# Performance work log

Measured on AMD Instinct MI355X. Metric: run time of the kernel, lower is better.

Reference implementation:

```python
import jax, jax.numpy as jnp
import numpy as np

B, G, N, E, F, H = 16, 8, 512, 8192, 128, 128
BN_EPS = 1e-5


def setup_inputs() -> dict:
    key = jax.random.key(0)
    ks = jax.random.split(key, 6)
    feats = jax.random.normal(ks[0], (B, G, N, F), jnp.float32)
    edges = jax.random.randint(ks[1], (B, G, 2, E), 0, N, dtype=jnp.int32)
    s = lambda k, shape: jax.random.normal(k, shape, jnp.float32) * 0.05
    return {
        "feats": feats,
        "edges": edges,
        "W0": s(ks[2], (F, H)), "b0": jnp.zeros((H,), jnp.float32),
        "W1": s(ks[3], (H, H)), "b1": jnp.zeros((H,), jnp.float32),
        "Wt": s(ks[4], (H, H)), "bt": jnp.zeros((H,), jnp.float32),
        "gamma": jnp.ones((H,), jnp.float32),
        "beta": jnp.zeros((H,), jnp.float32),
        "run_mean": jnp.zeros((H,), jnp.float32),
        "run_var": jnp.ones((H,), jnp.float32),
    }


def _gconv(x, src, dst, W, b):
    # DGL GraphConv with norm='both': relu(D_in^{-1/2} A D_out^{-1/2} X W + b)
    ones = jnp.ones(src.shape, jnp.float32)
    out_deg = jnp.clip(jax.ops.segment_sum(ones, src, num_segments=N), 1.0)
    in_deg = jnp.clip(jax.ops.segment_sum(ones, dst, num_segments=N), 1.0)
    h = x * jax.lax.rsqrt(out_deg)[:, None]          # src normalization
    agg = jax.ops.segment_sum(h[src], dst, num_segments=N)  # SpMM gather+scatter
    h = agg * jax.lax.rsqrt(in_deg)[:, None]          # dst normalization
    return jax.nn.relu(h @ W + b)


def reference(feats, edges, W0, b0, W1, b1, Wt, bt, gamma, beta, run_mean, run_var):
    def per_graph(x, e):
        src, dst = e[0], e[1]
        h = _gconv(x, src, dst, W0, b0)
        h = _gconv(h, src, dst, W1, b1)
        emb = h.mean(axis=0)  # dgl.mean_nodes readout -> [H]
        z = emb @ Wt + bt
        # BatchNorm1d in eval mode (batch of 1 graph embedding)
        z = gamma * (z - run_mean) * jax.lax.rsqrt(run_var + BN_EPS) + beta
        return jax.nn.relu(z)

    xf = feats.reshape(B * G, N, F)
    ef = edges.reshape(B * G, 2, E)
    out = jax.vmap(per_graph)(xf, ef)  # [B*G, H]
    # torch.stack nesting gives (batch, n_graph, 1, H) since mean_nodes returns [1, H]
    return out.reshape(B, G, 1, H)
```

## Files before the change

### kernel.cpp

```cpp
#include <hip/hip_runtime.h>
#include <hip/hip_bf16.h>

#define NN 512
#define NE 8192
#define NG 128
#define FH 128
#define APITCH 68
#define XPITCH 136
#define BN_EPS 1e-5f

typedef __attribute__((ext_vector_type(8))) short s8v;
typedef __attribute__((ext_vector_type(4))) float f4v;
typedef __attribute__((ext_vector_type(16))) float f16v;
typedef __attribute__((ext_vector_type(4))) unsigned short us4v;
typedef __attribute__((ext_vector_type(4))) unsigned int u4v;

__device__ inline unsigned short f2bf(float x) {
    unsigned u = __float_as_uint(x);
    unsigned r = (u + 0x7fffu + ((u >> 16) & 1u)) >> 16;
    return (unsigned short)r;
}
__device__ inline float bf2f(unsigned short h) { return __uint_as_float(((unsigned)h) << 16); }

__device__ inline unsigned bfpack(int f1bits, int f0bits) {
    return __builtin_amdgcn_perm((unsigned)f1bits, (unsigned)f0bits, 0x07060302u);
}

__global__ __launch_bounds__(1024) void k_build(const int* __restrict__ edges,
                                                float* __restrict__ rs_out,
                                                float* __restrict__ rs_in,
                                                int* __restrict__ bofs,
                                                unsigned short* __restrict__ epk,
                                                const float* __restrict__ W0,
                                                const float* __restrict__ W1,
                                                unsigned short* __restrict__ WP) {
    int g = blockIdx.x;
    int tid = threadIdx.x;

    if (g >= NG) {
        int which = g - NG;
        const float* W = which ? W1 : W0;
        for (int task = tid; task < 2048; task += 1024) {
            int t = task >> 6;
            int lane = task & 63;
            int nt = t >> 2, kk = t & 3;
            int n = nt * 16 + (lane & 15);
            int k0 = kk * 32 + (lane >> 4) * 8;
            unsigned short* dh = WP + ((size_t)which * 2 + 0) * 16384 + ((size_t)t * 64 + lane) * 8;
            unsigned short* dl = WP + ((size_t)which * 2 + 1) * 16384 + ((size_t)t * 64 + lane) * 8;
#pragma unroll
            for (int j = 0; j < 8; j++) {
                float v = W[(size_t)(k0 + j) * FH + n];
                unsigned short h = f2bf(v);
                dh[j] = h;
                dl[j] = f2bf(v - bf2f(h));
            }
        }
        return;
    }

    const int* src = edges + (size_t)g * 2 * NE;
    const int* dst = src + NE;

    __shared__ int degO[NN], degI[NN];
    __shared__ int scanA[1024], scanB[1024];
    __shared__ int fill[1024];
    __shared__ unsigned short pk[NE];

    for (int i = tid; i < NN; i += 1024) { degO[i] = 0; degI[i] = 0; }
    scanA[tid] = 0;
    __syncthreads();

    int rep = tid & 31;
    for (int u = tid; u < NE / 4; u += 1024) {
        int4 s = ((const int4*)src)[u];
        int4 d = ((const int4*)dst)[u];
        atomicAdd(&degO[s.x], 1); atomicAdd(&degO[s.y], 1);
        atomicAdd(&degO[s.z], 1); atomicAdd(&degO[s.w], 1);
        atomicAdd(&degI[d.x], 1); atomicAdd(&degI[d.y], 1);
        atomicAdd(&degI[d.z], 1); atomicAdd(&degI[d.w], 1);
        atomicAdd(&scanA[((((d.x >> 7) << 3) | (s.x >> 6)) << 5) + rep], 1);
        atomicAdd(&scanA[((((d.y >> 7) << 3) | (s.y >> 6)) << 5) + rep], 1);
        atomicAdd(&scanA[((((d.z >> 7) << 3) | (s.z >> 6)) << 5) + rep], 1);
        atomicAdd(&scanA[((((d.w >> 7) << 3) | (s.w >> 6)) << 5) + rep], 1);
    }
    __syncthreads();

    for (int i = tid; i < NN; i += 1024) {
        rs_out[g * NN + i] = rsqrtf((float)max(degO[i], 1));
        rs_in [g * NN + i] = rsqrtf((float)max(degI[i], 1));
    }

    int* sA = scanA; int* sB = scanB;
    for (int off = 1; off < 1024; off <<= 1) {
        int v = sA[tid];
        if (tid >= off) v += sA[tid - off];
        sB[tid] = v;
        __syncthreads();
        int* t = sA; sA = sB; sB = t;
    }
    int excl = tid ? sA[tid - 1] : 0;
    fill[tid] = excl;
    if ((tid & 31) == 0) bofs[g * 33 + (tid >> 5)] = excl;
    if (tid == 0) bofs[g * 33 + 32] = NE;
    __syncthreads();

    for (int u = tid; u < NE / 4; u += 1024) {
        int4 s = ((const int4*)src)[u];
        int4 d = ((const int4*)dst)[u];
        int c, p;
        c = ((((d.x >> 7) << 3) | (s.x >> 6)) << 5) + rep;
        p = atomicAdd(&fill[c], 1); pk[p] = (unsigned short)(((d.x & 127) << 6) | (s.x & 63));
        c = ((((d.y >> 7) << 3) | (s.y >> 6)) << 5) + rep;
        p = atomicAdd(&fill[c], 1); pk[p] = (unsigned short)(((d.y & 127) << 6) | (s.y & 63));
        c = ((((d.z >> 7) << 3) | (s.z >> 6)) << 5) + rep;
        p = atomicAdd(&fill[c], 1); pk[p] = (unsigned short)(((d.z & 127) << 6) | (s.z & 63));
        c = ((((d.w >> 7) << 3) | (s.w >> 6)) << 5) + rep;
        p = atomicAdd(&fill[c], 1); pk[p] = (unsigned short)(((d.w & 127) << 6) | (s.w & 63));
    }
    __syncthreads();
    ((int4*)(epk + (size_t)g * NE))[tid] = ((const int4*)pk)[tid];
}

__global__ __launch_bounds__(512) void k_packA(const int* __restrict__ bofs,
                                               const unsigned short* __restrict__ epk,
                                               unsigned short* __restrict__ AP) {
    int g = blockIdx.x, sb = blockIdx.y, tid = threadIdx.x;
    __shared__ float Af[128 * APITCH];
    __shared__ int bo_s[9];
    const unsigned short* ep = epk + (size_t)g * NE;
    unsigned short* Ag = AP + (size_t)g * 262144;

    if (tid < 9) bo_s[tid] = bofs[g * 33 + sb * 8 + tid];
    __syncthreads();
    int evNext = -1;
    { int e0 = bo_s[0] + tid; if (e0 < bo_s[1]) evNext = (int)ep[e0]; }

    for (int p = 0; p < 8; p++) {
        if (p) __syncthreads();
        float4 z4 = {0.f, 0.f, 0.f, 0.f};
        for (int i = tid; i < 128 * APITCH / 4; i += 512) ((float4*)Af)[i] = z4;
        __syncthreads();
        if (evNext >= 0) atomicAdd(&Af[(evNext >> 6) * APITCH + (evNext & 63)], 1.0f);
        for (int e = bo_s[p] + tid + 512; e < bo_s[p + 1]; e += 512) {
            int v = ep[e];
            atomicAdd(&Af[(v >> 6) * APITCH + (v & 63)], 1.0f);
        }
        __syncthreads();
        if (p < 7) { int e1 = bo_s[p + 1] + tid; evNext = (e1 < bo_s[p + 2]) ? (int)ep[e1] : -1; }
        else evNext = -1;
#pragma unroll
        for (int uu = 0; uu < 2; uu++) {
            int u = tid + uu * 512;
            int l31 = u & 31, lh = (u >> 5) & 1, Kl = (u >> 6) & 3, Rl = (u >> 8) & 3;
            const int4* ap = (const int4*)&Af[(Rl * 32 + l31) * APITCH + Kl * 16 + lh * 8];
            int4 a0 = ap[0], a1 = ap[1];
            u4v cv;
            cv.x = bfpack(a0.y, a0.x);
            cv.y = bfpack(a0.w, a0.z);
            cv.z = bfpack(a1.y, a1.x);
            cv.w = bfpack(a1.w, a1.z);
            int Rg = sb * 4 + Rl, K = p * 4 + Kl;
            *(u4v*)(Ag + (((size_t)(Rg * 32 + K) * 2 + lh) * 32 + l31) * 8) = cv;
        }
    }
}

__global__ __launch_bounds__(256) void k_gemm_f32(const float* __restrict__ X,
                                                  const unsigned short* __restrict__ WPh,
                                                  const unsigned short* __restrict__ WPl,
                                                  const float* __restrict__ rs,
                                                  unsigned short* __restrict__ Yf) {
    __shared__ unsigned short xh[64 * XPITCH];
    __shared__ unsigned short xl[64 * XPITCH];
    int tid = threadIdx.x;
    int sb = blockIdx.y;
    size_t r0 = (size_t)blockIdx.x * NN + (size_t)sb * 64;

    const float4* Xv = (const float4*)(X + r0 * FH);
#pragma unroll
    for (int i = 0; i < 8; i++) {
        int u = tid + i * 256;
        int row = u >> 5, c4 = (u & 31) * 4;
        float4 v = Xv[u];
        int off = row * XPITCH + c4;
        unsigned short h0 = f2bf(v.x), h1 = f2bf(v.y), h2 = f2bf(v.z), h3 = f2bf(v.w);
        us4v hv, lv;
        hv.x = h0; hv.y = h1; hv.z = h2; hv.w = h3;
        lv.x = f2bf(v.x - bf2f(h0));
        lv.y = f2bf(v.y - bf2f(h1));
        lv.z = f2bf(v.z - bf2f(h2));
        lv.w = f2bf(v.w - bf2f(h3));
        *(us4v*)(xh + off) = hv;
        *(us4v*)(xl + off) = lv;
    }
    __syncthreads();

    int lane = tid & 63, w = tid >> 6;
    int quad = lane >> 4, m = lane & 15;
    int arow = w * 16 + m;

    f4v acc[8];
#pragma unroll
    for (int nt = 0; nt < 8; nt++) acc[nt] = (f4v){0.f, 0.f, 0.f, 0.f};

#pragma unroll
    for (int kk = 0; kk < 4; kk++) {
        s8v ah = *(const s8v*)&xh[arow * XPITCH + kk * 32 + quad * 8];
        s8v al = *(const s8v*)&xl[arow * XPITCH + kk * 32 + quad * 8];
#pragma unroll
        for (int nt = 0; nt < 8; nt++) {
            s8v bh = *(const s8v*)(WPh + ((size_t)(nt * 4 + kk) * 64 + lane) * 8);
            s8v bl = *(const s8v*)(WPl + ((size_t)(nt * 4 + kk) * 64 + lane) * 8);
            acc[nt] = __builtin_amdgcn_mfma_f32_16x16x32_bf16(ah, bh, acc[nt], 0, 0, 0);
            acc[nt] = __builtin_amdgcn_mfma_f32_16x16x32_bf16(al, bh, acc[nt], 0, 0, 0);
            acc[nt] = __builtin_amdgcn_mfma_f32_16x16x32_bf16(ah, bl, acc[nt], 0, 0, 0);
        }
    }

    int orow = w * 16 + quad * 4;
    float4 rsv = *(const float4*)(rs + r0 + orow);
    int kb = sb * 4 + w, h2 = quad >> 1, j0 = (quad & 1) * 4;
    unsigned short* of = Yf + (size_t)blockIdx.x * (NN * FH);
#pragma unroll
    for (int nt = 0; nt < 8; nt++) {
        us4v v;
        v.x = f2bf(acc[nt][0] * rsv.x);
        v.y = f2bf(acc[nt][1] * rsv.y);
        v.z = f2bf(acc[nt][2] * rsv.z);
        v.w = f2bf(acc[nt][3] * rsv.w);
        *(us4v*)(of + ((size_t)(kb * 2 + h2) * 128 + nt * 16 + m) * 8 + j0) = v;
    }
}

__global__ __launch_bounds__(512) void k_fused(const unsigned short* __restrict__ Y1f,
                                               const unsigned short* __restrict__ AP,
                                               const float* __restrict__ rs_in,
                                               const float* __restrict__ rs_out,
                                               const float* __restrict__ bias,
                                               const unsigned short* __restrict__ WPh,
                                               const unsigned short* __restrict__ WPl,
                                               unsigned short* __restrict__ Y2f) {
    int g  = blockIdx.x;
    int sb = blockIdx.y;
    int tid = threadIdx.x;
    int lane = tid & 63, w8 = tid >> 6;
    int l31 = lane & 31, lh = lane >> 5;
    int mt = w8 & 3, nh = w8 >> 2;
    int base = sb * 128;

    __shared__ unsigned short hs[128 * XPITCH];
    __shared__ float rsin_s[128];

    if (tid < 128) rsin_s[tid] = rs_in[g * NN + base + tid];
    __syncthreads();

    const unsigned short* Yg = Y1f + (size_t)g * (NN * FH);
    const unsigned short* Ag = AP + (size_t)g * 262144;
    int Rg = sb * 4 + mt;
    int aoff  = Rg * 16384 + lh * 256 + l31 * 8;
    int boff0 = lh * 1024 + (nh * 64 + l31) * 8;
    int boff1 = boff0 + 256;

    f16v acc32[2];
#pragma unroll
    for (int t = 0; t < 2; t++)
#pragma unroll
        for (int i = 0; i < 16; i++) acc32[t][i] = 0.f;

    s8v aF[2][2], b0F[2][2], b1F[2][2];
    auto LD = [&](int buf, int Kb) {
#pragma unroll
        for (int q = 0; q < 2; q++) {
            int K = Kb + q;
            aF[buf][q]  = *(const s8v*)(Ag + aoff  + K * 512);
            b0F[buf][q] = *(const s8v*)(Yg + boff0 + K * 2048);
            b1F[buf][q] = *(const s8v*)(Yg + boff1 + K * 2048);
        }
    };
    LD(0, 0);
#pragma unroll
    for (int gq = 0; gq < 16; gq++) {
        int cur = gq & 1;
        if (gq < 15) LD(cur ^ 1, (gq + 1) * 2);
#pragma unroll
        for (int q = 0; q < 2; q++) {
            acc32[0] = __builtin_amdgcn_mfma_f32_32x32x16_bf16(aF[cur][q], b0F[cur][q], acc32[0], 0, 0, 0);
            acc32[1] = __builtin_amdgcn_mfma_f32_32x32x16_bf16(aF[cur][q], b1F[cur][q], acc32[1], 0, 0, 0);
        }
    }

#pragma unroll
    for (int t = 0; t < 2; t++) {
        int c = nh * 64 + t * 32 + l31;
        float bv = bias[c];
#pragma unroll
        for (int r = 0; r < 16; r++) {
            int row = mt * 32 + (r & 3) + 8 * (r >> 2) + 4 * lh;
            float hv = fmaxf(fmaf(rsin_s[row], acc32[t][r], bv), 0.f);
            hs[row * XPITCH + c] = f2bf(hv);
        }
    }
    __syncthreads();

    int quad = lane >> 4, m16 = lane & 15;
    f4v acc2[8];
#pragma unroll
    for (int nt = 0; nt < 8; nt++) acc2[nt] = (f4v){0.f, 0.f, 0.f, 0.f};

#pragma unroll
    for (int kk = 0; kk < 4; kk++) {
        s8v ah = *(const s8v*)&hs[(w8 * 16 + m16) * XPITCH + kk * 32 + quad * 8];
#pragma unroll
        for (int nt = 0; nt < 8; nt++) {
            s8v bh = *(const s8v*)(WPh + ((size_t)(nt * 4 + kk) * 64 + lane) * 8);
            s8v bl = *(const s8v*)(WPl + ((size_t)(nt * 4 + kk) * 64 + lane) * 8);
            acc2[nt] = __builtin_amdgcn_mfma_f32_16x16x32_bf16(ah, bh, acc2[nt], 0, 0, 0);
            acc2[nt] = __builtin_amdgcn_mfma_f32_16x16x32_bf16(ah, bl, acc2[nt], 0, 0, 0);
        }
    }

    int orow = w8 * 16 + quad * 4;
    float4 rsv = *(const float4*)(rs_out + (size_t)g * NN + base + orow);
    int kb = sb * 8 + w8, h2 = quad >> 1, j0 = (quad & 1) * 4;
    unsigned short* of = Y2f + (size_t)g * (NN * FH);
#pragma unroll
    for (int nt = 0; nt < 8; nt++) {
        us4v v;
        v.x = f2bf(acc2[nt][0] * rsv.x);
        v.y = f2bf(acc2[nt][1] * rsv.y);
        v.z = f2bf(acc2[nt][2] * rsv.z);
        v.w = f2bf(acc2[nt][3] * rsv.w);
        *(us4v*)(of + ((size_t)(kb * 2 + h2) * 128 + nt * 16 + m16) * 8 + j0) = v;
    }
}

__global__ __launch_bounds__(512) void k_gather_mean(const unsigned short* __restrict__ Y2f,
                                                     const unsigned short* __restrict__ AP,
                                                     const float* __restrict__ rs_in,
                                                     const float* __restrict__ bias,
                                                     float* __restrict__ partial) {
    int g  = blockIdx.x;
    int sb = blockIdx.y;
    int tid = threadIdx.x;
    int lane = tid & 63, w8 = tid >> 6;
    int l31 = lane & 31, lh = lane >> 5;
    int mt = w8 & 3, nh = w8 >> 2;
    int base = sb * 128;

    __shared__ float red[8 * 2 * 64];
    __shared__ float rsin_s[128];

    if (tid < 128) rsin_s[tid] = rs_in[g * NN + base + tid];
    __syncthreads();

    const unsigned short* Yg = Y2f + (size_t)g * (NN * FH);
    const unsigned short* Ag = AP + (size_t)g * 262144;
    int Rg = sb * 4 + mt;
    int aoff  = Rg * 16384 + lh * 256 + l31 * 8;
    int boff0 = lh * 1024 + (nh * 64 + l31) * 8;
    int boff1 = boff0 + 256;

    f16v acc32[2];
#pragma unroll
    for (int t = 0; t < 2; t++)
#pragma unroll
        for (int i = 0; i < 16; i++) acc32[t][i] = 0.f;

    s8v aF[2][2], b0F[2][2], b1F[2][2];
    auto LD = [&](int buf, int Kb) {
#pragma unroll
        for (int q = 0; q < 2; q++) {
            int K = Kb + q;
            aF[buf][q]  = *(const s8v*)(Ag + aoff  + K * 512);
            b0F[buf][q] = *(const s8v*)(Yg + boff0 + K * 2048);
            b1F[buf][q] = *(const s8v*)(Yg + boff1 + K * 2048);
        }
    };
    LD(0, 0);
#pragma unroll
    for (int gq = 0; gq < 16; gq++) {
        int cur = gq & 1;
        if (gq < 15) LD(cur ^ 1, (gq + 1) * 2);
#pragma unroll
        for (int q = 0; q < 2; q++) {
            acc32[0] = __builtin_amdgcn_mfma_f32_32x32x16_bf16(aF[cur][q], b0F[cur][q], acc32[0], 0, 0, 0);
            acc32[1] = __builtin_amdgcn_mfma_f32_32x32x16_bf16(aF[cur][q], b1F[cur][q], acc32[1], 0, 0, 0);
        }
    }

#pragma unroll
    for (int t = 0; t < 2; t++) {
        int c = nh * 64 + t * 32 + l31;
        float bv = bias[c];
        float s = 0.f;
#pragma unroll
        for (int r = 0; r < 16; r++) {
            int row = mt * 32 + (r & 3) + 8 * (r >> 2) + 4 * lh;
            s += fmaxf(fmaf(rsin_s[row], acc32[t][r], bv), 0.f);
        }
        red[(w8 * 2 + t) * 64 + lane] = s;
    }
    __syncthreads();
    if (tid < FH) {
        int f = tid;
        int nh2 = f >> 6, t2 = (f >> 5) & 1, cl = f & 31;
        float t = 0.f;
#pragma unroll
        for (int mtt = 0; mtt < 4; mtt++) {
            int w = nh2 * 4 + mtt;
            t += red[(w * 2 + t2) * 64 + cl] + red[(w * 2 + t2) * 64 + cl + 32];
        }
        partial[((size_t)g * 4 + sb) * FH + f] = t;
    }
}

__global__ __launch_bounds__(128) void k_head(const float* __restrict__ partial,
                                              const float* __restrict__ Wt,
                                              const float* __restrict__ bt,
                                              const float* __restrict__ gamma,
                                              const float* __restrict__ beta,
                                              const float* __restrict__ rmean,
                                              const float* __restrict__ rvar,
                                              float* __restrict__ out) {
    int g = blockIdx.x;
    int j = threadIdx.x;
    __shared__ float e[FH];
    float acc4 = 0.f;
#pragma unroll
    for (int q = 0; q < 4; q++) acc4 += partial[((size_t)g * 4 + q) * FH + j];
    e[j] = acc4 * (1.0f / (float)NN);
    __syncthreads();
    float acc = bt[j];
#pragma unroll 8
    for (int k = 0; k < FH; k++) acc += e[k] * Wt[(size_t)k * FH + j];
    float z = gamma[j] * (acc - rmean[j]) * rsqrtf(rvar[j] + BN_EPS) + beta[j];
    out[g * FH + j] = fmaxf(z, 0.f);
}

extern "C" void kernel_launch(void* const* d_in, const int* in_sizes, int n_in,
                              void* d_out, int out_size, void* d_ws, size_t ws_size,
                              hipStream_t stream) {
    const float* feats = (const float*)d_in[0];
    const int*   edges = (const int*)d_in[1];
    const float* W0    = (const float*)d_in[2];
    const float* b0    = (const float*)d_in[3];
    const float* W1    = (const float*)d_in[4];
    const float* b1    = (const float*)d_in[5];
    const float* Wt    = (const float*)d_in[6];
    const float* bt    = (const float*)d_in[7];
    const float* gamma = (const float*)d_in[8];
    const float* beta  = (const float*)d_in[9];
    const float* rmean = (const float*)d_in[10];
    const float* rvar  = (const float*)d_in[11];
    float* out = (float*)d_out;

    char* w = (char*)d_ws;
    float* rs_out  = (float*)w;   w += sizeof(float) * NG * NN;
    float* rs_in   = (float*)w;   w += sizeof(float) * NG * NN;
    int*   bofs    = (int*)w;     w += sizeof(int) * NG * 33;
    unsigned short* epk = (unsigned short*)w; w += sizeof(unsigned short) * (size_t)NG * NE;
    unsigned short* WP  = (unsigned short*)w; w += sizeof(unsigned short) * 4 * 16384;
    unsigned short* Y1  = (unsigned short*)w; w += sizeof(unsigned short) * (size_t)NG * NN * FH;
    unsigned short* Y2  = (unsigned short*)w; w += sizeof(unsigned short) * (size_t)NG * NN * FH;
    unsigned short* AP  = (unsigned short*)w; w += sizeof(unsigned short) * (size_t)NG * 262144;
    float* partial = (float*)w;   w += sizeof(float) * NG * 4 * FH;

    unsigned short* WPh0 = WP;
    unsigned short* WPl0 = WP + 16384;
    unsigned short* WPh1 = WP + 32768;
    unsigned short* WPl1 = WP + 49152;

    k_build<<<NG + 2, 1024, 0, stream>>>(edges, rs_out, rs_in, bofs, epk, W0, W1, WP);

    k_packA<<<dim3(NG, 4), 512, 0, stream>>>(bofs, epk, AP);

    k_gemm_f32<<<dim3(NG, 8), 256, 0, stream>>>(feats, WPh0, WPl0, rs_out, Y1);

    k_fused<<<dim3(NG, 4), 512, 0, stream>>>(Y1, AP, rs_in, rs_out, b0, WPh1, WPl1, Y2);

    k_gather_mean<<<dim3(NG, 4), 512, 0, stream>>>(Y2, AP, rs_in, b1, partial);

    k_head<<<NG, 128, 0, stream>>>(partial, Wt, bt, gamma, beta, rmean, rvar, out);

    (void)in_sizes; (void)n_in; (void)out_size; (void)ws_size;
}
```

Measured before the change: 185.3 us.

## Use 2x2 MFMA register tiles with deeper prefetch in aggregation kernels

Aggregation kernels k_fused and k_gather_mean now run with 256 threads per block instead of 512. Each wave computes a 2x2 block of 32x32 output tiles, so every A and B fragment loaded from global memory is used by two MFMAs, and a 6-deep register ring keeps loads in flight. The second-layer weight GEMM in k_fused switches to 32x32x16 MFMAs, with W1 repacked into a matching layout in k_build. This cuts global fragment loads per MFMA and increases latency hiding, at the cost of much higher register pressure (launch_bounds 256,2) and half as many waves per block.

```diff
diff --git a/kernel.cpp b/kernel.cpp
--- a/kernel.cpp
+++ b/kernel.cpp
@@ -39,21 +39,37 @@
 
     if (g >= NG) {
         int which = g - NG;
-        const float* W = which ? W1 : W0;
-        for (int task = tid; task < 2048; task += 1024) {
-            int t = task >> 6;
-            int lane = task & 63;
-            int nt = t >> 2, kk = t & 3;
-            int n = nt * 16 + (lane & 15);
-            int k0 = kk * 32 + (lane >> 4) * 8;
-            unsigned short* dh = WP + ((size_t)which * 2 + 0) * 16384 + ((size_t)t * 64 + lane) * 8;
-            unsigned short* dl = WP + ((size_t)which * 2 + 1) * 16384 + ((size_t)t * 64 + lane) * 8;
-#pragma unroll
-            for (int j = 0; j < 8; j++) {
-                float v = W[(size_t)(k0 + j) * FH + n];
-                unsigned short h = f2bf(v);
-                dh[j] = h;
-                dl[j] = f2bf(v - bf2f(h));
+        if (which == 0) {
+            for (int task = tid; task < 2048; task += 1024) {
+                int t = task >> 6;
+                int lane = task & 63;
+                int nt = t >> 2, kk = t & 3;
+                int n = nt * 16 + (lane & 15);
+                int k0 = kk * 32 + (lane >> 4) * 8;
+                unsigned short* dh = WP + ((size_t)t * 64 + lane) * 8;
+                unsigned short* dl = WP + 16384 + ((size_t)t * 64 + lane) * 8;
+#pragma unroll
+                for (int j = 0; j < 8; j++) {
+                    float v = W0[(size_t)(k0 + j) * FH + n];
+                    unsigned short h = f2bf(v);
+                    dh[j] = h;
+                    dl[j] = f2bf(v - bf2f(h));
+                }
+            }
+        } else {
+            for (int task = tid; task < 2048; task += 1024) {
+                int kk = task >> 8;
+                int rem = task & 255;
+                int lhp = rem >> 7, c = rem & 127;
+                unsigned short* dh = WP + 2 * 16384 + ((size_t)((kk * 2 + lhp) * 128 + c)) * 8;
+                unsigned short* dl = WP + 3 * 16384 + ((size_t)((kk * 2 + lhp) * 128 + c)) * 8;
+#pragma unroll
+                for (int j = 0; j < 8; j++) {
+                    float v = W1[(size_t)(kk * 16 + lhp * 8 + j) * FH + c];
+                    unsigned short h = f2bf(v);
+                    dh[j] = h;
+                    dl[j] = f2bf(v - bf2f(h));
+                }
             }
         }
         return;
@@ -233,161 +249,162 @@
     }
 }
 
-__global__ __launch_bounds__(512) void k_fused(const unsigned short* __restrict__ Y1f,
-                                               const unsigned short* __restrict__ AP,
-                                               const float* __restrict__ rs_in,
-                                               const float* __restrict__ rs_out,
-                                               const float* __restrict__ bias,
-                                               const unsigned short* __restrict__ WPh,
-                                               const unsigned short* __restrict__ WPl,
-                                               unsigned short* __restrict__ Y2f) {
+__global__ __launch_bounds__(256, 2) void k_fused(const unsigned short* __restrict__ Y1f,
+                                                  const unsigned short* __restrict__ AP,
+                                                  const float* __restrict__ rs_in,
+                                                  const float* __restrict__ rs_out,
+                                                  const float* __restrict__ bias,
+                                                  const unsigned short* __restrict__ W32h,
+                                                  const unsigned short* __restrict__ W32l,
+                                                  unsigned short* __restrict__ Y2f) {
     int g  = blockIdx.x;
     int sb = blockIdx.y;
     int tid = threadIdx.x;
-    int lane = tid & 63, w8 = tid >> 6;
+    int lane = tid & 63, w4 = tid >> 6;
     int l31 = lane & 31, lh = lane >> 5;
-    int mt = w8 & 3, nh = w8 >> 2;
+    int nh = w4 >> 1, mq = w4 & 1;
     int base = sb * 128;
 
     __shared__ unsigned short hs[128 * XPITCH];
     __shared__ float rsin_s[128];
 
     if (tid < 128) rsin_s[tid] = rs_in[g * NN + base + tid];
-    __syncthreads();
 
     const unsigned short* Yg = Y1f + (size_t)g * (NN * FH);
     const unsigned short* Ag = AP + (size_t)g * 262144;
-    int Rg = sb * 4 + mt;
-    int aoff  = Rg * 16384 + lh * 256 + l31 * 8;
-    int boff0 = lh * 1024 + (nh * 64 + l31) * 8;
-    int boff1 = boff0 + 256;
-
-    f16v acc32[2];
-#pragma unroll
-    for (int t = 0; t < 2; t++)
-#pragma unroll
-        for (int i = 0; i < 16; i++) acc32[t][i] = 0.f;
-
-    s8v aF[2][2], b0F[2][2], b1F[2][2];
-    auto LD = [&](int buf, int Kb) {
-#pragma unroll
-        for (int q = 0; q < 2; q++) {
-            int K = Kb + q;
-            aF[buf][q]  = *(const s8v*)(Ag + aoff  + K * 512);
-            b0F[buf][q] = *(const s8v*)(Yg + boff0 + K * 2048);
-            b1F[buf][q] = *(const s8v*)(Yg + boff1 + K * 2048);
-        }
+    int aoff = (sb * 4 + mq * 2) * 16384 + lh * 256 + l31 * 8;
+    int boff = lh * 1024 + (nh * 64 + l31) * 8;
+
+    f16v a00, a01, a10, a11;
+#pragma unroll
+    for (int i = 0; i < 16; i++) { a00[i] = 0.f; a01[i] = 0.f; a10[i] = 0.f; a11[i] = 0.f; }
+
+    s8v aF[6][2], bF[6][2];
+    auto LD = [&](int buf, int K) {
+        aF[buf][0] = *(const s8v*)(Ag + aoff + K * 512);
+        aF[buf][1] = *(const s8v*)(Ag + aoff + 16384 + K * 512);
+        bF[buf][0] = *(const s8v*)(Yg + boff + K * 2048);
+        bF[buf][1] = *(const s8v*)(Yg + boff + 256 + K * 2048);
     };
-    LD(0, 0);
-#pragma unroll
-    for (int gq = 0; gq < 16; gq++) {
-        int cur = gq & 1;
-        if (gq < 15) LD(cur ^ 1, (gq + 1) * 2);
-#pragma unroll
-        for (int q = 0; q < 2; q++) {
-            acc32[0] = __builtin_amdgcn_mfma_f32_32x32x16_bf16(aF[cur][q], b0F[cur][q], acc32[0], 0, 0, 0);
-            acc32[1] = __builtin_amdgcn_mfma_f32_32x32x16_bf16(aF[cur][q], b1F[cur][q], acc32[1], 0, 0, 0);
-        }
-    }
-
-#pragma unroll
-    for (int t = 0; t < 2; t++) {
-        int c = nh * 64 + t * 32 + l31;
-        float bv = bias[c];
-#pragma unroll
-        for (int r = 0; r < 16; r++) {
-            int row = mt * 32 + (r & 3) + 8 * (r >> 2) + 4 * lh;
-            float hv = fmaxf(fmaf(rsin_s[row], acc32[t][r], bv), 0.f);
-            hs[row * XPITCH + c] = f2bf(hv);
-        }
-    }
-    __syncthreads();
-
-    int quad = lane >> 4, m16 = lane & 15;
-    f4v acc2[8];
-#pragma unroll
-    for (int nt = 0; nt < 8; nt++) acc2[nt] = (f4v){0.f, 0.f, 0.f, 0.f};
-
-#pragma unroll
-    for (int kk = 0; kk < 4; kk++) {
-        s8v ah = *(const s8v*)&hs[(w8 * 16 + m16) * XPITCH + kk * 32 + quad * 8];
-#pragma unroll
-        for (int nt = 0; nt < 8; nt++) {
-            s8v bh = *(const s8v*)(WPh + ((size_t)(nt * 4 + kk) * 64 + lane) * 8);
-            s8v bl = *(const s8v*)(WPl + ((size_t)(nt * 4 + kk) * 64 + lane) * 8);
-            acc2[nt] = __builtin_amdgcn_mfma_f32_16x16x32_bf16(ah, bh, acc2[nt], 0, 0, 0);
-            acc2[nt] = __builtin_amdgcn_mfma_f32_16x16x32_bf16(ah, bl, acc2[nt], 0, 0, 0);
-        }
-    }
-
-    int orow = w8 * 16 + quad * 4;
-    float4 rsv = *(const float4*)(rs_out + (size_t)g * NN + base + orow);
-    int kb = sb * 8 + w8, h2 = quad >> 1, j0 = (quad & 1) * 4;
+    LD(0, 0); LD(1, 1); LD(2, 2); LD(3, 3); LD(4, 4); LD(5, 5);
+#pragma unroll
+    for (int k = 0; k < 32; k++) {
+        int cur = k % 6;
+        a00 = __builtin_amdgcn_mfma_f32_32x32x16_bf16(aF[cur][0], bF[cur][0], a00, 0, 0, 0);
+        a01 = __builtin_amdgcn_mfma_f32_32x32x16_bf16(aF[cur][0], bF[cur][1], a01, 0, 0, 0);
+        a10 = __builtin_amdgcn_mfma_f32_32x32x16_bf16(aF[cur][1], bF[cur][0], a10, 0, 0, 0);
+        a11 = __builtin_amdgcn_mfma_f32_32x32x16_bf16(aF[cur][1], bF[cur][1], a11, 0, 0, 0);
+        if (k + 6 < 32) LD(cur, k + 6);
+    }
+    __syncthreads();
+
+#define EPI1(ACC, Rl, t)                                                        \
+    {                                                                           \
+        int c = nh * 64 + (t) * 32 + l31;                                       \
+        float bv = bias[c];                                                     \
+        _Pragma("unroll")                                                       \
+        for (int r = 0; r < 16; r++) {                                          \
+            int row = (mq * 2 + (Rl)) * 32 + (r & 3) + 8 * (r >> 2) + 4 * lh;   \
+            float hv = fmaxf(fmaf(rsin_s[row], (ACC)[r], bv), 0.f);             \
+            hs[row * XPITCH + c] = f2bf(hv);                                    \
+        }                                                                       \
+    }
+    EPI1(a00, 0, 0) EPI1(a01, 0, 1) EPI1(a10, 1, 0) EPI1(a11, 1, 1)
+#undef EPI1
+    __syncthreads();
+
+    f16v acc2[2][2];
+#pragma unroll
+    for (int q = 0; q < 2; q++)
+#pragma unroll
+        for (int t = 0; t < 2; t++)
+#pragma unroll
+            for (int i = 0; i < 16; i++) acc2[q][t][i] = 0.f;
+
+#pragma unroll
+    for (int kk = 0; kk < 8; kk++) {
+        s8v a0 = *(const s8v*)&hs[((mq * 2 + 0) * 32 + l31) * XPITCH + kk * 16 + lh * 8];
+        s8v a1 = *(const s8v*)&hs[((mq * 2 + 1) * 32 + l31) * XPITCH + kk * 16 + lh * 8];
+#pragma unroll
+        for (int t = 0; t < 2; t++) {
+            int c = nh * 64 + t * 32 + l31;
+            s8v bh = *(const s8v*)(W32h + ((size_t)((kk * 2 + lh) * 128 + c)) * 8);
+            s8v bl = *(const s8v*)(W32l + ((size_t)((kk * 2 + lh) * 128 + c)) * 8);
+            acc2[0][t] = __builtin_amdgcn_mfma_f32_32x32x16_bf16(a0, bh, acc2[0][t], 0, 0, 0);
+            acc2[0][t] = __builtin_amdgcn_mfma_f32_32x32x16_bf16(a0, bl, acc2[0][t], 0, 0, 0);
+            acc2[1][t] = __builtin_amdgcn_mfma_f32_32x32x16_bf16(a1, bh, acc2[1][t], 0, 0, 0);
+            acc2[1][t] = __builtin_amdgcn_mfma_f32_32x32x16_bf16(a1, bl, acc2[1][t], 0, 0, 0);
+        }
+    }
+
     unsigned short* of = Y2f + (size_t)g * (NN * FH);
 #pragma unroll
-    for (int nt = 0; nt < 8; nt++) {
-        us4v v;
-        v.x = f2bf(acc2[nt][0] * rsv.x);
-        v.y = f2bf(acc2[nt][1] * rsv.y);
-        v.z = f2bf(acc2[nt][2] * rsv.z);
-        v.w = f2bf(acc2[nt][3] * rsv.w);
-        *(us4v*)(of + ((size_t)(kb * 2 + h2) * 128 + nt * 16 + m16) * 8 + j0) = v;
-    }
-}
-
-__global__ __launch_bounds__(512) void k_gather_mean(const unsigned short* __restrict__ Y2f,
-                                                     const unsigned short* __restrict__ AP,
-                                                     const float* __restrict__ rs_in,
-                                                     const float* __restrict__ bias,
-                                                     float* __restrict__ partial) {
+    for (int q = 0; q < 2; q++) {
+        int Rgl = mq * 2 + q;
+#pragma unroll
+        for (int t = 0; t < 2; t++) {
+            int c = nh * 64 + t * 32 + l31;
+#pragma unroll
+            for (int rq = 0; rq < 4; rq++) {
+                int n0 = base + Rgl * 32 + 8 * rq + 4 * lh;
+                float4 rsv = *(const float4*)(rs_out + (size_t)g * NN + n0);
+                int kb = n0 >> 4, lhb = (n0 >> 3) & 1, j0 = n0 & 7;
+                us4v v;
+                v.x = f2bf(acc2[q][t][rq * 4 + 0] * rsv.x);
+                v.y = f2bf(acc2[q][t][rq * 4 + 1] * rsv.y);
+                v.z = f2bf(acc2[q][t][rq * 4 + 2] * rsv.z);
+                v.w = f2bf(acc2[q][t][rq * 4 + 3] * rsv.w);
+                *(us4v*)(of + ((size_t)(kb * 2 + lhb) * 128 + c) * 8 + j0) = v;
+            }
+        }
+    }
+}
+
+__global__ __launch_bounds__(256, 2) void k_gather_mean(const unsigned short* __restrict__ Y2f,
+                                                        const unsigned short* __restrict__ AP,
+                                                        const float* __restrict__ rs_in,
+                                                        const float* __restrict__ bias,
+                                                        float* __restrict__ partial) {
     int g  = blockIdx.x;
     int sb = blockIdx.y;
     int tid = threadIdx.x;
-    int lane = tid & 63, w8 = tid >> 6;
+    int lane = tid & 63, w4 = tid >> 6;
     int l31 = lane & 31, lh = lane >> 5;
-    int mt = w8 & 3, nh = w8 >> 2;
+    int nh = w4 >> 1, mq = w4 & 1;
     int base = sb * 128;
 
-    __shared__ float red[8 * 2 * 64];
+    __shared__ float red[4 * 2 * 64];
     __shared__ float rsin_s[128];
 
     if (tid < 128) rsin_s[tid] = rs_in[g * NN + base + tid];
-    __syncthreads();
 
     const unsigned short* Yg = Y2f + (size_t)g * (NN * FH);
     const unsigned short* Ag = AP + (size_t)g * 262144;
-    int Rg = sb * 4 + mt;
-    int aoff  = Rg * 16384 + lh * 256 + l31 * 8;
-    int boff0 = lh * 1024 + (nh * 64 + l31) * 8;
-    int boff1 = boff0 + 256;
-
-    f16v acc32[2];
-#pragma unroll
-    for (int t = 0; t < 2; t++)
-#pragma unroll
-        for (int i = 0; i < 16; i++) acc32[t][i] = 0.f;
-
-    s8v aF[2][2], b0F[2][2], b1F[2][2];
-    auto LD = [&](int buf, int Kb) {
-#pragma unroll
-        for (int q = 0; q < 2; q++) {
-            int K = Kb + q;
-            aF[buf][q]  = *(const s8v*)(Ag + aoff  + K * 512);
-            b0F[buf][q] = *(const s8v*)(Yg + boff0 + K * 2048);
-            b1F[buf][q] = *(const s8v*)(Yg + boff1 + K * 2048);
-        }
+    int aoff = (sb * 4 + mq * 2) * 16384 + lh * 256 + l31 * 8;
+    int boff = lh * 1024 + (nh * 64 + l31) * 8;
+
+    f16v a00, a01, a10, a11;
+#pragma unroll
+    for (int i = 0; i < 16; i++) { a00[i] = 0.f; a01[i] = 0.f; a10[i] = 0.f; a11[i] = 0.f; }
+
+    s8v aF[6][2], bF[6][2];
+    auto LD = [&](int buf, int K) {
+        aF[buf][0] = *(const s8v*)(Ag + aoff + K * 512);
+        aF[buf][1] = *(const s8v*)(Ag + aoff + 16384 + K * 512);
+        bF[buf][0] = *(const s8v*)(Yg + boff + K * 2048);
+        bF[buf][1] = *(const s8v*)(Yg + boff + 256 + K * 2048);
     };
-    LD(0, 0);
-#pragma unroll
-    for (int gq = 0; gq < 16; gq++) {
-        int cur = gq & 1;
-        if (gq < 15) LD(cur ^ 1, (gq + 1) * 2);
-#pragma unroll
-        for (int q = 0; q < 2; q++) {
-            acc32[0] = __builtin_amdgcn_mfma_f32_32x32x16_bf16(aF[cur][q], b0F[cur][q], acc32[0], 0, 0, 0);
-            acc32[1] = __builtin_amdgcn_mfma_f32_32x32x16_bf16(aF[cur][q], b1F[cur][q], acc32[1], 0, 0, 0);
-        }
-    }
+    LD(0, 0); LD(1, 1); LD(2, 2); LD(3, 3); LD(4, 4); LD(5, 5);
+#pragma unroll
+    for (int k = 0; k < 32; k++) {
+        int cur = k % 6;
+        a00 = __builtin_amdgcn_mfma_f32_32x32x16_bf16(aF[cur][0], bF[cur][0], a00, 0, 0, 0);
+        a01 = __builtin_amdgcn_mfma_f32_32x32x16_bf16(aF[cur][0], bF[cur][1], a01, 0, 0, 0);
+        a10 = __builtin_amdgcn_mfma_f32_32x32x16_bf16(aF[cur][1], bF[cur][0], a10, 0, 0, 0);
+        a11 = __builtin_amdgcn_mfma_f32_32x32x16_bf16(aF[cur][1], bF[cur][1], a11, 0, 0, 0);
+        if (k + 6 < 32) LD(cur, k + 6);
+    }
+    __syncthreads();
 
 #pragma unroll
     for (int t = 0; t < 2; t++) {
@@ -396,10 +413,14 @@
         float s = 0.f;
 #pragma unroll
         for (int r = 0; r < 16; r++) {
-            int row = mt * 32 + (r & 3) + 8 * (r >> 2) + 4 * lh;
-            s += fmaxf(fmaf(rsin_s[row], acc32[t][r], bv), 0.f);
-        }
-        red[(w8 * 2 + t) * 64 + lane] = s;
+            int row0 = (mq * 2 + 0) * 32 + (r & 3) + 8 * (r >> 2) + 4 * lh;
+            int row1 = (mq * 2 + 1) * 32 + (r & 3) + 8 * (r >> 2) + 4 * lh;
+            float v0 = (t == 0) ? a00[r] : a01[r];
+            float v1 = (t == 0) ? a10[r] : a11[r];
+            s += fmaxf(fmaf(rsin_s[row0], v0, bv), 0.f);
+            s += fmaxf(fmaf(rsin_s[row1], v1, bv), 0.f);
+        }
+        red[(w4 * 2 + t) * 64 + lane] = s;
     }
     __syncthreads();
     if (tid < FH) {
@@ -407,8 +428,8 @@
         int nh2 = f >> 6, t2 = (f >> 5) & 1, cl = f & 31;
         float t = 0.f;
 #pragma unroll
-        for (int mtt = 0; mtt < 4; mtt++) {
-            int w = nh2 * 4 + mtt;
+        for (int mqq = 0; mqq < 2; mqq++) {
+            int w = nh2 * 2 + mqq;
             t += red[(w * 2 + t2) * 64 + cl] + red[(w * 2 + t2) * 64 + cl + 32];
         }
         partial[((size_t)g * 4 + sb) * FH + f] = t;
@@ -468,8 +489,8 @@
 
     unsigned short* WPh0 = WP;
     unsigned short* WPl0 = WP + 16384;
-    unsigned short* WPh1 = WP + 32768;
-    unsigned short* WPl1 = WP + 49152;
+    unsigned short* W32h = WP + 32768;
+    unsigned short* W32l = WP + 49152;
 
     k_build<<<NG + 2, 1024, 0, stream>>>(edges, rs_out, rs_in, bofs, epk, W0, W1, WP);
 
@@ -477,9 +498,9 @@
 
     k_gemm_f32<<<dim3(NG, 8), 256, 0, stream>>>(feats, WPh0, WPl0, rs_out, Y1);
 
-    k_fused<<<dim3(NG, 4), 512, 0, stream>>>(Y1, AP, rs_in, rs_out, b0, WPh1, WPl1, Y2);
-
-    k_gather_mean<<<dim3(NG, 4), 512, 0, stream>>>(Y2, AP, rs_in, b1, partial);
+    k_fused<<<dim3(NG, 4), 256, 0, stream>>>(Y1, AP, rs_in, rs_out, b0, W32h, W32l, Y2);
+
+    k_gather_mean<<<dim3(NG, 4), 256, 0, stream>>>(Y2, AP, rs_in, b1, partial);
 
     k_head<<<NG, 128, 0, stream>>>(partial, Wt, bt, gamma, beta, rmean, rvar, out);
 
```

Result: faster. 180.4 us (-2.6%).
